# Kernel optimization log

Measured on AMD Instinct MI355X. Metric: run time of the kernel, lower is better.

The kernel has to match this reference:

```python
import jax, jax.numpy as jnp
import numpy as np

NEG_INF = -1e9  # additive mask value for masked softmax


def setup_inputs() -> dict:
    key = jax.random.key(0)
    k1, k2, k3, k4, k5 = jax.random.split(key, 5)
    bz, rv_num, rv_len, in_feat, out_feat = 32, 10, 128, 300, 128
    seq_a = jax.random.normal(k1, (bz, rv_num, rv_len, in_feat), dtype=jnp.float32)
    seq_b = jax.random.normal(k2, (bz, rv_num, rv_len, in_feat), dtype=jnp.float32)
    mask_a = jax.random.randint(k3, (bz, rv_num, rv_len), 0, 2, dtype=jnp.int32)
    mask_b = jax.random.randint(k4, (bz, rv_num, rv_len), 0, 2, dtype=jnp.int32)
    # guarantee at least one valid position per review (avoid fully-masked rows)
    mask_a = mask_a.at[:, :, 0].set(1)
    mask_b = mask_b.at[:, :, 0].set(1)
    # FC transform params (xavier-normal-ish weight, zero bias)
    W = jax.random.normal(k5, (in_feat, out_feat), dtype=jnp.float32) * (2.0 / np.sqrt(in_feat + out_feat))
    b = jnp.zeros((out_feat,), dtype=jnp.float32)
    return {"seq_a": seq_a, "seq_b": seq_b, "mask_a": mask_a, "mask_b": mask_b, "W": W, "b": b}


def _masked_softmax(scores, mask):
    # scores: [N, L], mask: [N, L] in {0,1}
    logits = jnp.where(mask > 0, scores, NEG_INF)
    return jax.nn.softmax(logits, axis=-1)


def reference(seq_a, seq_b, mask_a, mask_b, W, b):
    bz, rv_num, rv_len, _ = seq_a.shape
    hdim = W.shape[1]
    N = bz * rv_num          # flattened batch of reviews
    M = rv_num * rv_len      # all tokens on the other side

    # FC + ReLU feature transform
    ta = jax.nn.relu(jnp.einsum('bnld,dh->bnlh', seq_a, W) + b)
    tb = jax.nn.relu(jnp.einsum('bnld,dh->bnlh', seq_b, W) + b)

    sa = ta.reshape(N, rv_len, hdim)
    sb = tb.reshape(N, rv_len, hdim)
    # expand: each review attends over ALL tokens of the other sequence in its sample
    ea = jnp.broadcast_to(ta.reshape(bz, 1, M, hdim), (bz, rv_num, M, hdim)).reshape(N, M, hdim)
    eb = jnp.broadcast_to(tb.reshape(bz, 1, M, hdim), (bz, rv_num, M, hdim)).reshape(N, M, hdim)

    # DOT interaction (no scale): affinity [N, rv_len, M]
    atob_aff = jnp.einsum('nld,nmd->nlm', sa, eb)
    btoa_aff = jnp.einsum('nld,nmd->nlm', sb, ea)

    # MEAN pooling over the other-sequence axis
    atob_scores = atob_aff.mean(axis=-1)  # [N, rv_len]
    btoa_scores = btoa_aff.mean(axis=-1)

    ma = mask_a.reshape(N, rv_len)
    mb = mask_b.reshape(N, rv_len)
    atob_w = _masked_softmax(atob_scores, ma)
    btoa_w = _masked_softmax(btoa_scores, mb)

    a_out = jnp.einsum('nl,nld->nd', atob_w, sa)
    b_out = jnp.einsum('nl,nld->nd', btoa_w, sb)
    return (a_out, b_out, atob_w, btoa_w)
```

## Files before the change

### kernel.cpp

```cpp
#include <hip/hip_runtime.h>
#include <hip/hip_bf16.h>


#define K_FEAT 300
#define H 128
#define NTOK 40960
#define NREV 320
#define TOK_PER_SAMPLE 1280
#define TM 64
#define FC_BLKS_PER_SIDE 640
#define FC_BLKS_PER_SAMPLE 20
#define NCHUNK 10
#define WFRAG_ELEMS (NCHUNK * 4 * 4 * 64 * 8)

typedef __attribute__((ext_vector_type(8))) short bf16x8;
typedef __attribute__((ext_vector_type(4))) float f32x4;
typedef unsigned short u16;
typedef unsigned int u32;

static __device__ __forceinline__ u16 f2bf(float x) {
    u32 u = __float_as_uint(x);
    return (u16)((u + 0x7fffu + ((u >> 16) & 1u)) >> 16);
}
static __device__ __forceinline__ float bf2f(u16 s) {
    return __uint_as_float(((u32)s) << 16);
}

__global__ void wsplit_kernel(const float* __restrict__ W, u16* __restrict__ Wfrag)
{
    int i = blockIdx.x * 256 + threadIdx.x;
    if (i >= WFRAG_ELEMS) return;
    int j    = i & 7;
    int lane = (i >> 3) & 63;
    int frag = (i >> 9) & 3;
    int wave = (i >> 11) & 3;
    int c    = i >> 13;
    int nn = lane & 15, quad = lane >> 4;
    int t2 = frag >> 1, part = frag & 1;
    int h = (2 * wave + t2) * 16 + nn;
    int k = c * 32 + quad * 8 + j;
    float w = (k < K_FEAT) ? W[(size_t)k * H + h] : 0.f;
    u16 hi = f2bf(w);
    Wfrag[i] = part ? f2bf(w - bf2f(hi)) : hi;
}

static __device__ __forceinline__ void cvt_pack(const float4 a, const float4 b,
                                                uint4& hp, uint4& lp)
{
    u16 h0 = f2bf(a.x), h1 = f2bf(a.y), h2 = f2bf(a.z), h3 = f2bf(a.w);
    u16 h4 = f2bf(b.x), h5 = f2bf(b.y), h6 = f2bf(b.z), h7 = f2bf(b.w);
    hp.x = (u32)h0 | ((u32)h1 << 16);
    hp.y = (u32)h2 | ((u32)h3 << 16);
    hp.z = (u32)h4 | ((u32)h5 << 16);
    hp.w = (u32)h6 | ((u32)h7 << 16);
    lp.x = (u32)f2bf(a.x - bf2f(h0)) | ((u32)f2bf(a.y - bf2f(h1)) << 16);
    lp.y = (u32)f2bf(a.z - bf2f(h2)) | ((u32)f2bf(a.w - bf2f(h3)) << 16);
    lp.z = (u32)f2bf(b.x - bf2f(h4)) | ((u32)f2bf(b.y - bf2f(h5)) << 16);
    lp.w = (u32)f2bf(b.z - bf2f(h6)) | ((u32)f2bf(b.w - bf2f(h7)) << 16);
}

__global__ __launch_bounds__(256, 5) void fc_mfma_kernel(
    const float* __restrict__ seq_a, const float* __restrict__ seq_b,
    const u16* __restrict__ Wfrag, const float* __restrict__ bias,
    u16* __restrict__ ta, u16* __restrict__ tb,
    float* __restrict__ psum_a, float* __restrict__ psum_b)
{
    __shared__ __align__(16) u16 Ah_s[2][4 * 512];
    __shared__ __align__(16) u16 Al_s[2][4 * 512];
    __shared__ float bias_s[H];

    int blk = blockIdx.x;
    const float* seq; u16* outp; float* psum;
    if (blk < FC_BLKS_PER_SIDE) { seq = seq_a; outp = ta; psum = psum_a; }
    else { seq = seq_b; outp = tb; psum = psum_b; blk -= FC_BLKS_PER_SIDE; }

    const int tid = threadIdx.x;
    const int tok0 = blk * TM;
    const int wave = tid >> 6;
    const int lane = tid & 63;
    const int nn = lane & 15;
    const int quad = lane >> 4;

    if (tid < H) bias_s[tid] = bias[tid];

    const int st_tok = tid >> 2;
    const int st_q = tid & 3;
    const float* srow = seq + (size_t)(tok0 + st_tok) * K_FEAT + st_q * 8;
    const int stg = (st_tok >> 4) * 512 + ((st_q << 4) + (st_tok & 15)) * 8;

    f32x4 acc[4][2];
#pragma unroll
    for (int m = 0; m < 4; ++m) {
        acc[m][0] = (f32x4){0.f, 0.f, 0.f, 0.f};
        acc[m][1] = (f32x4){0.f, 0.f, 0.f, 0.f};
    }

#define LOADC(cc, x0, x1) do {                                  \
        int kchk = (cc) * 32 + st_q * 8;                        \
        x0 = make_float4(0.f, 0.f, 0.f, 0.f);                   \
        x1 = make_float4(0.f, 0.f, 0.f, 0.f);                   \
        if (kchk + 4 <= K_FEAT) x0 = *(const float4*)(srow + (cc) * 32);     \
        if (kchk + 8 <= K_FEAT) x1 = *(const float4*)(srow + (cc) * 32 + 4); \
    } while (0)

#define STOREC(bufi, x0, x1) do {                               \
        uint4 hp, lp;                                           \
        cvt_pack(x0, x1, hp, lp);                               \
        *(uint4*)&Ah_s[bufi][stg] = hp;                         \
        *(uint4*)&Al_s[bufi][stg] = lp;                         \
    } while (0)

    float4 a0, a1, b0, b1;
    LOADC(0, a0, a1);
    LOADC(1, b0, b1);
    STOREC(0, a0, a1);
    __syncthreads();

#pragma unroll
    for (int c = 0; c < NCHUNK; ++c) {
        const int cur = c & 1;
        if (c + 2 < NCHUNK) {
            if ((c & 1) == 0) { LOADC(c + 2, a0, a1); }
            else              { LOADC(c + 2, b0, b1); }
        }
        const u16* wf = Wfrag + (size_t)(c * 4 + wave) * 2048;
        bf16x8 bh0 = *(const bf16x8*)&wf[0 * 512 + lane * 8];
        bf16x8 bl0 = *(const bf16x8*)&wf[1 * 512 + lane * 8];
        bf16x8 bh1 = *(const bf16x8*)&wf[2 * 512 + lane * 8];
        bf16x8 bl1 = *(const bf16x8*)&wf[3 * 512 + lane * 8];
#pragma unroll
        for (int m = 0; m < 4; ++m) {
            bf16x8 a_hi = *(const bf16x8*)&Ah_s[cur][m * 512 + lane * 8];
            bf16x8 a_lo = *(const bf16x8*)&Al_s[cur][m * 512 + lane * 8];
            acc[m][0] = __builtin_amdgcn_mfma_f32_16x16x32_bf16(bh0, a_hi, acc[m][0], 0, 0, 0);
            acc[m][0] = __builtin_amdgcn_mfma_f32_16x16x32_bf16(bl0, a_hi, acc[m][0], 0, 0, 0);
            acc[m][0] = __builtin_amdgcn_mfma_f32_16x16x32_bf16(bh0, a_lo, acc[m][0], 0, 0, 0);
            acc[m][1] = __builtin_amdgcn_mfma_f32_16x16x32_bf16(bh1, a_hi, acc[m][1], 0, 0, 0);
            acc[m][1] = __builtin_amdgcn_mfma_f32_16x16x32_bf16(bl1, a_hi, acc[m][1], 0, 0, 0);
            acc[m][1] = __builtin_amdgcn_mfma_f32_16x16x32_bf16(bh1, a_lo, acc[m][1], 0, 0, 0);
        }
        if (c + 1 < NCHUNK) {
            if ((c & 1) == 0) { STOREC(cur ^ 1, b0, b1); }
            else              { STOREC(cur ^ 1, a0, a1); }
            __syncthreads();
        }
    }
#undef LOADC
#undef STOREC

#pragma unroll
    for (int ht = 0; ht < 2; ++ht) {
        int h0 = (2 * wave + ht) * 16 + quad * 4;
        float4 bb = *(const float4*)&bias_s[h0];
        float fs[4] = {0.f, 0.f, 0.f, 0.f};
#pragma unroll
        for (int tt = 0; tt < 4; ++tt) {
            int tok = tok0 + tt * 16 + nn;
            float v0 = fmaxf(acc[tt][ht][0] + bb.x, 0.f);
            float v1 = fmaxf(acc[tt][ht][1] + bb.y, 0.f);
            float v2 = fmaxf(acc[tt][ht][2] + bb.z, 0.f);
            float v3 = fmaxf(acc[tt][ht][3] + bb.w, 0.f);
            fs[0] += v0; fs[1] += v1; fs[2] += v2; fs[3] += v3;
            uint2 p;
            p.x = (u32)f2bf(v0) | ((u32)f2bf(v1) << 16);
            p.y = (u32)f2bf(v2) | ((u32)f2bf(v3) << 16);
            *(uint2*)&outp[(size_t)tok * H + h0] = p;
        }
#pragma unroll
        for (int r = 0; r < 4; ++r) {
            fs[r] += __shfl_xor(fs[r], 1);
            fs[r] += __shfl_xor(fs[r], 2);
            fs[r] += __shfl_xor(fs[r], 4);
            fs[r] += __shfl_xor(fs[r], 8);
        }
        if (nn == 0) {
#pragma unroll
            for (int r = 0; r < 4; ++r)
                psum[(size_t)blk * H + h0 + r] = fs[r];
        }
    }
}

__global__ __launch_bounds__(512) void attn_kernel(
    const u16* __restrict__ ta, const u16* __restrict__ tb,
    const int* __restrict__ mask_a, const int* __restrict__ mask_b,
    const float* __restrict__ psum_a, const float* __restrict__ psum_b,
    float* __restrict__ out)
{
    int n = blockIdx.x;
    int side = 0;
    if (n >= NREV) { side = 1; n -= NREV; }

    const u16* t = side ? tb : ta;
    const int* mask = side ? mask_b : mask_a;
    const float* psum_o = side ? psum_a : psum_b;
    float* out_vec = out + (side ? NREV * H : 0);
    float* out_w = out + 2 * NREV * H + (side ? NREV * H : 0);

    int sample = n / 10;
    int tid = threadIdx.x;

    __shared__ float score_part[128 * 17];
    __shared__ float mean_s[128];
    __shared__ float w_s[128];
    __shared__ float red[8];
    __shared__ float part_out[32 * 128];

    if (tid < 128) {
        float s = 0.f;
        const float* pb = psum_o + (size_t)sample * FC_BLKS_PER_SAMPLE * H + tid;
#pragma unroll
        for (int i = 0; i < FC_BLKS_PER_SAMPLE; ++i) s += pb[(size_t)i * H];
        mean_s[tid] = s * (1.0f / (float)TOK_PER_SAMPLE);
    }
    __syncthreads();

    const u16* rowbase = t + (size_t)n * 128 * H;

#pragma unroll
    for (int i = 0; i < 4; ++i) {
        int q = tid + 512 * i;
        int r = q >> 4;
        int c8 = q & 15;
        uint4 v = *(const uint4*)&rowbase[r * H + c8 * 8];
        const float* m = &mean_s[c8 * 8];
        float p = 0.f;
        p += bf2f((u16)(v.x & 0xffff)) * m[0];
        p += bf2f((u16)(v.x >> 16)) * m[1];
        p += bf2f((u16)(v.y & 0xffff)) * m[2];
        p += bf2f((u16)(v.y >> 16)) * m[3];
        p += bf2f((u16)(v.z & 0xffff)) * m[4];
        p += bf2f((u16)(v.z >> 16)) * m[5];
        p += bf2f((u16)(v.w & 0xffff)) * m[6];
        p += bf2f((u16)(v.w >> 16)) * m[7];
        score_part[r * 17 + c8] = p;
    }
    __syncthreads();

    float logit = -1e9f;
    if (tid < 128) {
        float s = 0.f;
#pragma unroll
        for (int j = 0; j < 16; ++j) s += score_part[tid * 17 + j];
        int mv = mask[n * 128 + tid];
        logit = (mv > 0) ? s : -1e9f;
    }

    float mx = logit;
    for (int off = 32; off > 0; off >>= 1) mx = fmaxf(mx, __shfl_xor(mx, off));
    if ((tid & 63) == 0) red[tid >> 6] = mx;
    __syncthreads();
    mx = red[0];
#pragma unroll
    for (int rr = 1; rr < 8; ++rr) mx = fmaxf(mx, red[rr]);
    __syncthreads();

    float e = __expf(logit - mx);
    float ssum = e;
    for (int off = 32; off > 0; off >>= 1) ssum += __shfl_xor(ssum, off);
    if ((tid & 63) == 0) red[tid >> 6] = ssum;
    __syncthreads();
    ssum = 0.f;
#pragma unroll
    for (int rr = 0; rr < 8; ++rr) ssum += red[rr];

    float w = e / ssum;
    if (tid < 128) {
        w_s[tid] = w;
        out_w[n * 128 + tid] = w;
    }
    __syncthreads();

    int c8 = tid & 15;
    int lp = tid >> 4;
    float o[8] = {0.f, 0.f, 0.f, 0.f, 0.f, 0.f, 0.f, 0.f};
#pragma unroll
    for (int k = 0; k < 4; ++k) {
        int l = k * 32 + lp;
        float wl = w_s[l];
        uint4 v = *(const uint4*)&rowbase[l * H + c8 * 8];
        o[0] = fmaf(wl, bf2f((u16)(v.x & 0xffff)), o[0]);
        o[1] = fmaf(wl, bf2f((u16)(v.x >> 16)), o[1]);
        o[2] = fmaf(wl, bf2f((u16)(v.y & 0xffff)), o[2]);
        o[3] = fmaf(wl, bf2f((u16)(v.y >> 16)), o[3]);
        o[4] = fmaf(wl, bf2f((u16)(v.z & 0xffff)), o[4]);
        o[5] = fmaf(wl, bf2f((u16)(v.z >> 16)), o[5]);
        o[6] = fmaf(wl, bf2f((u16)(v.w & 0xffff)), o[6]);
        o[7] = fmaf(wl, bf2f((u16)(v.w >> 16)), o[7]);
    }
    *(float4*)&part_out[lp * 128 + c8 * 8] = make_float4(o[0], o[1], o[2], o[3]);
    *(float4*)&part_out[lp * 128 + c8 * 8 + 4] = make_float4(o[4], o[5], o[6], o[7]);
    __syncthreads();
    if (tid < 128) {
        float s = 0.f;
#pragma unroll
        for (int p = 0; p < 32; ++p) s += part_out[p * 128 + tid];
        out_vec[n * 128 + tid] = s;
    }
}

extern "C" void kernel_launch(void* const* d_in, const int* in_sizes, int n_in,
                              void* d_out, int out_size, void* d_ws, size_t ws_size,
                              hipStream_t stream)
{
    const float* seq_a = (const float*)d_in[0];
    const float* seq_b = (const float*)d_in[1];
    const int* mask_a = (const int*)d_in[2];
    const int* mask_b = (const int*)d_in[3];
    const float* W = (const float*)d_in[4];
    const float* bias = (const float*)d_in[5];
    float* out = (float*)d_out;

    u16* ta = (u16*)d_ws;
    u16* tb = ta + (size_t)NTOK * H;
    float* psum_a = (float*)(tb + (size_t)NTOK * H);
    float* psum_b = psum_a + FC_BLKS_PER_SIDE * H;
    u16* Wfrag = (u16*)(psum_b + FC_BLKS_PER_SIDE * H);

    wsplit_kernel<<<(WFRAG_ELEMS + 255) / 256, 256, 0, stream>>>(W, Wfrag);
    fc_mfma_kernel<<<2 * FC_BLKS_PER_SIDE, 256, 0, stream>>>(seq_a, seq_b, Wfrag, bias, ta, tb, psum_a, psum_b);
    attn_kernel<<<640, 512, 0, stream>>>(ta, tb, mask_a, mask_b, psum_a, psum_b, out);
}
```

Baseline: 152.8 us.

## Make each FC wave own a private 16-token tile and drop block barriers

The FC kernel now gives each wave its own 16 tokens across all 128 output features, each with private double-buffered LDS staging. This removes every __syncthreads from the K loop. Partial column sums are written per wave, so there are four times as many psum groups, and the attention kernel reduces 80 partials per sample with four accumulators. In exchange, each wave now loads all of the W fragments from global/L2 memory, which is four times the W traffic, and it uses more accumulator registers.

```diff
diff --git a/kernel.cpp b/kernel.cpp
--- a/kernel.cpp
+++ b/kernel.cpp
@@ -9,7 +9,8 @@
 #define TOK_PER_SAMPLE 1280
 #define TM 64
 #define FC_BLKS_PER_SIDE 640
-#define FC_BLKS_PER_SAMPLE 20
+#define PSUM_GROUPS 2560
+#define PSUM_PER_SAMPLE 80
 #define NCHUNK 10
 #define WFRAG_ELEMS (NCHUNK * 4 * 4 * 64 * 8)
 
@@ -33,11 +34,11 @@
     int j    = i & 7;
     int lane = (i >> 3) & 63;
     int frag = (i >> 9) & 3;
-    int wave = (i >> 11) & 3;
+    int p    = (i >> 11) & 3;
     int c    = i >> 13;
     int nn = lane & 15, quad = lane >> 4;
     int t2 = frag >> 1, part = frag & 1;
-    int h = (2 * wave + t2) * 16 + nn;
+    int h = (2 * p + t2) * 16 + nn;
     int k = c * 32 + quad * 8 + j;
     float w = (k < K_FEAT) ? W[(size_t)k * H + h] : 0.f;
     u16 hi = f2bf(w);
@@ -65,9 +66,8 @@
     u16* __restrict__ ta, u16* __restrict__ tb,
     float* __restrict__ psum_a, float* __restrict__ psum_b)
 {
-    __shared__ __align__(16) u16 Ah_s[2][4 * 512];
-    __shared__ __align__(16) u16 Al_s[2][4 * 512];
-    __shared__ float bias_s[H];
+    __shared__ __align__(16) u16 Ah_s[4][2][512];
+    __shared__ __align__(16) u16 Al_s[4][2][512];
 
     int blk = blockIdx.x;
     const float* seq; u16* outp; float* psum;
@@ -75,46 +75,45 @@
     else { seq = seq_b; outp = tb; psum = psum_b; blk -= FC_BLKS_PER_SIDE; }
 
     const int tid = threadIdx.x;
-    const int tok0 = blk * TM;
     const int wave = tid >> 6;
     const int lane = tid & 63;
     const int nn = lane & 15;
     const int quad = lane >> 4;
-
-    if (tid < H) bias_s[tid] = bias[tid];
-
-    const int st_tok = tid >> 2;
-    const int st_q = tid & 3;
-    const float* srow = seq + (size_t)(tok0 + st_tok) * K_FEAT + st_q * 8;
-    const int stg = (st_tok >> 4) * 512 + ((st_q << 4) + (st_tok & 15)) * 8;
-
-    f32x4 acc[4][2];
-#pragma unroll
-    for (int m = 0; m < 4; ++m) {
-        acc[m][0] = (f32x4){0.f, 0.f, 0.f, 0.f};
-        acc[m][1] = (f32x4){0.f, 0.f, 0.f, 0.f};
-    }
-
-#define LOADC(cc, x0, x1) do {                                  \
-        int kchk = (cc) * 32 + st_q * 8;                        \
-        x0 = make_float4(0.f, 0.f, 0.f, 0.f);                   \
-        x1 = make_float4(0.f, 0.f, 0.f, 0.f);                   \
-        if (kchk + 4 <= K_FEAT) x0 = *(const float4*)(srow + (cc) * 32);     \
-        if (kchk + 8 <= K_FEAT) x1 = *(const float4*)(srow + (cc) * 32 + 4); \
+    const int tok0w = blk * TM + wave * 16;
+
+    const int ts = lane >> 2;
+    const int qs = lane & 3;
+    const float* srow = seq + (size_t)(tok0w + ts) * K_FEAT + qs * 8;
+    const int stg = ((qs << 4) + ts) * 8;
+
+    f32x4 acc[8];
+#pragma unroll
+    for (int t = 0; t < 8; ++t) acc[t] = (f32x4){0.f, 0.f, 0.f, 0.f};
+
+#define LOADC(cc, x0, x1) do {                                                \
+        if ((cc) < 9) {   \
+            x0 = *(const float4*)(srow + (cc) * 32);                          \
+            x1 = *(const float4*)(srow + (cc) * 32 + 4);                      \
+        } else {                                                              \
+            int kb = (cc) * 32 + qs * 8;                                      \
+            x0 = make_float4(0.f, 0.f, 0.f, 0.f);                             \
+            x1 = make_float4(0.f, 0.f, 0.f, 0.f);                             \
+            if (kb + 4 <= K_FEAT) x0 = *(const float4*)(srow + (cc) * 32);    \
+            if (kb + 8 <= K_FEAT) x1 = *(const float4*)(srow + (cc) * 32 + 4);\
+        }                                                                     \
     } while (0)
 
 #define STOREC(bufi, x0, x1) do {                               \
         uint4 hp, lp;                                           \
         cvt_pack(x0, x1, hp, lp);                               \
-        *(uint4*)&Ah_s[bufi][stg] = hp;                         \
-        *(uint4*)&Al_s[bufi][stg] = lp;                         \
+        *(uint4*)&Ah_s[wave][bufi][stg] = hp;                   \
+        *(uint4*)&Al_s[wave][bufi][stg] = lp;                   \
     } while (0)
 
     float4 a0, a1, b0, b1;
     LOADC(0, a0, a1);
     LOADC(1, b0, b1);
     STOREC(0, a0, a1);
-    __syncthreads();
 
 #pragma unroll
     for (int c = 0; c < NCHUNK; ++c) {
@@ -123,60 +122,57 @@
             if ((c & 1) == 0) { LOADC(c + 2, a0, a1); }
             else              { LOADC(c + 2, b0, b1); }
         }
-        const u16* wf = Wfrag + (size_t)(c * 4 + wave) * 2048;
-        bf16x8 bh0 = *(const bf16x8*)&wf[0 * 512 + lane * 8];
-        bf16x8 bl0 = *(const bf16x8*)&wf[1 * 512 + lane * 8];
-        bf16x8 bh1 = *(const bf16x8*)&wf[2 * 512 + lane * 8];
-        bf16x8 bl1 = *(const bf16x8*)&wf[3 * 512 + lane * 8];
-#pragma unroll
-        for (int m = 0; m < 4; ++m) {
-            bf16x8 a_hi = *(const bf16x8*)&Ah_s[cur][m * 512 + lane * 8];
-            bf16x8 a_lo = *(const bf16x8*)&Al_s[cur][m * 512 + lane * 8];
-            acc[m][0] = __builtin_amdgcn_mfma_f32_16x16x32_bf16(bh0, a_hi, acc[m][0], 0, 0, 0);
-            acc[m][0] = __builtin_amdgcn_mfma_f32_16x16x32_bf16(bl0, a_hi, acc[m][0], 0, 0, 0);
-            acc[m][0] = __builtin_amdgcn_mfma_f32_16x16x32_bf16(bh0, a_lo, acc[m][0], 0, 0, 0);
-            acc[m][1] = __builtin_amdgcn_mfma_f32_16x16x32_bf16(bh1, a_hi, acc[m][1], 0, 0, 0);
-            acc[m][1] = __builtin_amdgcn_mfma_f32_16x16x32_bf16(bl1, a_hi, acc[m][1], 0, 0, 0);
-            acc[m][1] = __builtin_amdgcn_mfma_f32_16x16x32_bf16(bh1, a_lo, acc[m][1], 0, 0, 0);
-        }
+        bf16x8 a_hi = *(const bf16x8*)&Ah_s[wave][cur][lane * 8];
+        bf16x8 a_lo = *(const bf16x8*)&Al_s[wave][cur][lane * 8];
         if (c + 1 < NCHUNK) {
             if ((c & 1) == 0) { STOREC(cur ^ 1, b0, b1); }
             else              { STOREC(cur ^ 1, a0, a1); }
-            __syncthreads();
+        }
+        const u16* wfc = Wfrag + (size_t)c * 8192;
+#pragma unroll
+        for (int p = 0; p < 4; ++p) {
+            const u16* wf = wfc + p * 2048;
+            bf16x8 bh0 = *(const bf16x8*)&wf[0 * 512 + lane * 8];
+            bf16x8 bl0 = *(const bf16x8*)&wf[1 * 512 + lane * 8];
+            bf16x8 bh1 = *(const bf16x8*)&wf[2 * 512 + lane * 8];
+            bf16x8 bl1 = *(const bf16x8*)&wf[3 * 512 + lane * 8];
+            acc[2 * p]     = __builtin_amdgcn_mfma_f32_16x16x32_bf16(bh0, a_hi, acc[2 * p], 0, 0, 0);
+            acc[2 * p]     = __builtin_amdgcn_mfma_f32_16x16x32_bf16(bl0, a_hi, acc[2 * p], 0, 0, 0);
+            acc[2 * p]     = __builtin_amdgcn_mfma_f32_16x16x32_bf16(bh0, a_lo, acc[2 * p], 0, 0, 0);
+            acc[2 * p + 1] = __builtin_amdgcn_mfma_f32_16x16x32_bf16(bh1, a_hi, acc[2 * p + 1], 0, 0, 0);
+            acc[2 * p + 1] = __builtin_amdgcn_mfma_f32_16x16x32_bf16(bl1, a_hi, acc[2 * p + 1], 0, 0, 0);
+            acc[2 * p + 1] = __builtin_amdgcn_mfma_f32_16x16x32_bf16(bh1, a_lo, acc[2 * p + 1], 0, 0, 0);
         }
     }
 #undef LOADC
 #undef STOREC
 
-#pragma unroll
-    for (int ht = 0; ht < 2; ++ht) {
-        int h0 = (2 * wave + ht) * 16 + quad * 4;
-        float4 bb = *(const float4*)&bias_s[h0];
-        float fs[4] = {0.f, 0.f, 0.f, 0.f};
-#pragma unroll
-        for (int tt = 0; tt < 4; ++tt) {
-            int tok = tok0 + tt * 16 + nn;
-            float v0 = fmaxf(acc[tt][ht][0] + bb.x, 0.f);
-            float v1 = fmaxf(acc[tt][ht][1] + bb.y, 0.f);
-            float v2 = fmaxf(acc[tt][ht][2] + bb.z, 0.f);
-            float v3 = fmaxf(acc[tt][ht][3] + bb.w, 0.f);
-            fs[0] += v0; fs[1] += v1; fs[2] += v2; fs[3] += v3;
-            uint2 p;
-            p.x = (u32)f2bf(v0) | ((u32)f2bf(v1) << 16);
-            p.y = (u32)f2bf(v2) | ((u32)f2bf(v3) << 16);
-            *(uint2*)&outp[(size_t)tok * H + h0] = p;
-        }
-#pragma unroll
-        for (int r = 0; r < 4; ++r) {
-            fs[r] += __shfl_xor(fs[r], 1);
-            fs[r] += __shfl_xor(fs[r], 2);
-            fs[r] += __shfl_xor(fs[r], 4);
-            fs[r] += __shfl_xor(fs[r], 8);
+    const int g = blk * 4 + wave;
+#pragma unroll
+    for (int ht = 0; ht < 8; ++ht) {
+        const int h0 = ht * 16 + quad * 4;
+        const float4 bb = *(const float4*)&bias[h0];
+        float v0 = fmaxf(acc[ht][0] + bb.x, 0.f);
+        float v1 = fmaxf(acc[ht][1] + bb.y, 0.f);
+        float v2 = fmaxf(acc[ht][2] + bb.z, 0.f);
+        float v3 = fmaxf(acc[ht][3] + bb.w, 0.f);
+        uint2 pk;
+        pk.x = (u32)f2bf(v0) | ((u32)f2bf(v1) << 16);
+        pk.y = (u32)f2bf(v2) | ((u32)f2bf(v3) << 16);
+        *(uint2*)&outp[(size_t)(tok0w + nn) * H + h0] = pk;
+        float fs0 = v0, fs1 = v1, fs2 = v2, fs3 = v3;
+#pragma unroll
+        for (int x = 1; x < 16; x <<= 1) {
+            fs0 += __shfl_xor(fs0, x);
+            fs1 += __shfl_xor(fs1, x);
+            fs2 += __shfl_xor(fs2, x);
+            fs3 += __shfl_xor(fs3, x);
         }
         if (nn == 0) {
-#pragma unroll
-            for (int r = 0; r < 4; ++r)
-                psum[(size_t)blk * H + h0 + r] = fs[r];
+            psum[(size_t)g * H + h0 + 0] = fs0;
+            psum[(size_t)g * H + h0 + 1] = fs1;
+            psum[(size_t)g * H + h0 + 2] = fs2;
+            psum[(size_t)g * H + h0 + 3] = fs3;
         }
     }
 }
@@ -207,11 +203,16 @@
     __shared__ float part_out[32 * 128];
 
     if (tid < 128) {
-        float s = 0.f;
-        const float* pb = psum_o + (size_t)sample * FC_BLKS_PER_SAMPLE * H + tid;
-#pragma unroll
-        for (int i = 0; i < FC_BLKS_PER_SAMPLE; ++i) s += pb[(size_t)i * H];
-        mean_s[tid] = s * (1.0f / (float)TOK_PER_SAMPLE);
+        const float* pb = psum_o + (size_t)sample * PSUM_PER_SAMPLE * H + tid;
+        float s0 = 0.f, s1 = 0.f, s2 = 0.f, s3 = 0.f;
+#pragma unroll
+        for (int i = 0; i < PSUM_PER_SAMPLE; i += 4) {
+            s0 += pb[(size_t)(i + 0) * H];
+            s1 += pb[(size_t)(i + 1) * H];
+            s2 += pb[(size_t)(i + 2) * H];
+            s3 += pb[(size_t)(i + 3) * H];
+        }
+        mean_s[tid] = (s0 + s1 + s2 + s3) * (1.0f / (float)TOK_PER_SAMPLE);
     }
     __syncthreads();
 
@@ -314,8 +315,8 @@
     u16* ta = (u16*)d_ws;
     u16* tb = ta + (size_t)NTOK * H;
     float* psum_a = (float*)(tb + (size_t)NTOK * H);
-    float* psum_b = psum_a + FC_BLKS_PER_SIDE * H;
-    u16* Wfrag = (u16*)(psum_b + FC_BLKS_PER_SIDE * H);
+    float* psum_b = psum_a + PSUM_GROUPS * H;
+    u16* Wfrag = (u16*)(psum_b + PSUM_GROUPS * H);
 
     wsplit_kernel<<<(WFRAG_ELEMS + 255) / 256, 256, 0, stream>>>(W, Wfrag);
     fc_mfma_kernel<<<2 * FC_BLKS_PER_SIDE, 256, 0, stream>>>(seq_a, seq_b, Wfrag, bias, ta, tb, psum_a, psum_b);
```

After: 190.8 us. +24.9%, slower.

## Replace split-bf16 triple MFMA with single fp16 MFMA; cache rows in LDS

Applied to the files above, without the earlier changes.

The FC GEMM drops the hi/lo bf16 split, which took three MFMAs per tile, and instead converts activations and weights to fp16 for a single f16 MFMA. This cuts MFMA count, LDS traffic and conversion work, at the cost of fp16 precision and range on the inputs. The load prefetch depth drops from two chunks to one, and bias is read from global memory directly. The attention kernel now stages each review's token rows in LDS on the first pass so the second pass reads LDS instead of global memory, and it reuses one float buffer for both reduction scratch arrays.

```diff
diff --git a/kernel.cpp b/kernel.cpp
--- a/kernel.cpp
+++ b/kernel.cpp
@@ -11,9 +11,10 @@
 #define FC_BLKS_PER_SIDE 640
 #define FC_BLKS_PER_SAMPLE 20
 #define NCHUNK 10
-#define WFRAG_ELEMS (NCHUNK * 4 * 4 * 64 * 8)
-
-typedef __attribute__((ext_vector_type(8))) short bf16x8;
+#define WFRAG_ELEMS (NCHUNK * 4 * 2 * 64 * 8)
+
+typedef _Float16 f16;
+typedef __attribute__((ext_vector_type(8))) _Float16 f16x8;
 typedef __attribute__((ext_vector_type(4))) float f32x4;
 typedef unsigned short u16;
 typedef unsigned int u32;
@@ -24,6 +25,13 @@
 }
 static __device__ __forceinline__ float bf2f(u16 s) {
     return __uint_as_float(((u32)s) << 16);
+}
+static __device__ __forceinline__ u16 f2h_bits(float x) {
+    f16 h = (f16)x;
+    return *(u16*)&h;
+}
+static __device__ __forceinline__ u32 pk2h(float a, float b) {
+    return (u32)f2h_bits(a) | ((u32)f2h_bits(b) << 16);
 }
 
 __global__ void wsplit_kernel(const float* __restrict__ W, u16* __restrict__ Wfrag)
@@ -32,31 +40,14 @@
     if (i >= WFRAG_ELEMS) return;
     int j    = i & 7;
     int lane = (i >> 3) & 63;
-    int frag = (i >> 9) & 3;
-    int wave = (i >> 11) & 3;
-    int c    = i >> 13;
+    int t2   = (i >> 9) & 1;
+    int p    = (i >> 10) & 3;
+    int c    = i >> 12;
     int nn = lane & 15, quad = lane >> 4;
-    int t2 = frag >> 1, part = frag & 1;
-    int h = (2 * wave + t2) * 16 + nn;
+    int h = (2 * p + t2) * 16 + nn;
     int k = c * 32 + quad * 8 + j;
     float w = (k < K_FEAT) ? W[(size_t)k * H + h] : 0.f;
-    u16 hi = f2bf(w);
-    Wfrag[i] = part ? f2bf(w - bf2f(hi)) : hi;
-}
-
-static __device__ __forceinline__ void cvt_pack(const float4 a, const float4 b,
-                                                uint4& hp, uint4& lp)
-{
-    u16 h0 = f2bf(a.x), h1 = f2bf(a.y), h2 = f2bf(a.z), h3 = f2bf(a.w);
-    u16 h4 = f2bf(b.x), h5 = f2bf(b.y), h6 = f2bf(b.z), h7 = f2bf(b.w);
-    hp.x = (u32)h0 | ((u32)h1 << 16);
-    hp.y = (u32)h2 | ((u32)h3 << 16);
-    hp.z = (u32)h4 | ((u32)h5 << 16);
-    hp.w = (u32)h6 | ((u32)h7 << 16);
-    lp.x = (u32)f2bf(a.x - bf2f(h0)) | ((u32)f2bf(a.y - bf2f(h1)) << 16);
-    lp.y = (u32)f2bf(a.z - bf2f(h2)) | ((u32)f2bf(a.w - bf2f(h3)) << 16);
-    lp.z = (u32)f2bf(b.x - bf2f(h4)) | ((u32)f2bf(b.y - bf2f(h5)) << 16);
-    lp.w = (u32)f2bf(b.z - bf2f(h6)) | ((u32)f2bf(b.w - bf2f(h7)) << 16);
+    Wfrag[i] = f2h_bits(w);
 }
 
 __global__ __launch_bounds__(256, 5) void fc_mfma_kernel(
@@ -65,9 +56,7 @@
     u16* __restrict__ ta, u16* __restrict__ tb,
     float* __restrict__ psum_a, float* __restrict__ psum_b)
 {
-    __shared__ __align__(16) u16 Ah_s[2][4 * 512];
-    __shared__ __align__(16) u16 Al_s[2][4 * 512];
-    __shared__ float bias_s[H];
+    __shared__ __align__(16) u16 A_s[2][4 * 512];
 
     int blk = blockIdx.x;
     const float* seq; u16* outp; float* psum;
@@ -81,8 +70,6 @@
     const int nn = lane & 15;
     const int quad = lane >> 4;
 
-    if (tid < H) bias_s[tid] = bias[tid];
-
     const int st_tok = tid >> 2;
     const int st_q = tid & 3;
     const float* srow = seq + (size_t)(tok0 + st_tok) * K_FEAT + st_q * 8;
@@ -95,53 +82,48 @@
         acc[m][1] = (f32x4){0.f, 0.f, 0.f, 0.f};
     }
 
-#define LOADC(cc, x0, x1) do {                                  \
-        int kchk = (cc) * 32 + st_q * 8;                        \
-        x0 = make_float4(0.f, 0.f, 0.f, 0.f);                   \
-        x1 = make_float4(0.f, 0.f, 0.f, 0.f);                   \
-        if (kchk + 4 <= K_FEAT) x0 = *(const float4*)(srow + (cc) * 32);     \
-        if (kchk + 8 <= K_FEAT) x1 = *(const float4*)(srow + (cc) * 32 + 4); \
+#define LOADC(cc, x0, x1) do {                                                \
+        if ((cc) < 9) {        \
+            x0 = *(const float4*)(srow + (cc) * 32);                          \
+            x1 = *(const float4*)(srow + (cc) * 32 + 4);                      \
+        } else {                                                              \
+            int kb = (cc) * 32 + st_q * 8;                                    \
+            x0 = make_float4(0.f, 0.f, 0.f, 0.f);                             \
+            x1 = make_float4(0.f, 0.f, 0.f, 0.f);                             \
+            if (kb + 4 <= K_FEAT) x0 = *(const float4*)(srow + (cc) * 32);    \
+            if (kb + 8 <= K_FEAT) x1 = *(const float4*)(srow + (cc) * 32 + 4);\
+        }                                                                     \
     } while (0)
 
 #define STOREC(bufi, x0, x1) do {                               \
-        uint4 hp, lp;                                           \
-        cvt_pack(x0, x1, hp, lp);                               \
-        *(uint4*)&Ah_s[bufi][stg] = hp;                         \
-        *(uint4*)&Al_s[bufi][stg] = lp;                         \
+        uint4 pkt;                                              \
+        pkt.x = pk2h(x0.x, x0.y);                               \
+        pkt.y = pk2h(x0.z, x0.w);                               \
+        pkt.z = pk2h(x1.x, x1.y);                               \
+        pkt.w = pk2h(x1.z, x1.w);                               \
+        *(uint4*)&A_s[bufi][stg] = pkt;                         \
     } while (0)
 
-    float4 a0, a1, b0, b1;
-    LOADC(0, a0, a1);
-    LOADC(1, b0, b1);
-    STOREC(0, a0, a1);
+    float4 x0, x1;
+    LOADC(0, x0, x1);
+    STOREC(0, x0, x1);
     __syncthreads();
 
 #pragma unroll
     for (int c = 0; c < NCHUNK; ++c) {
         const int cur = c & 1;
-        if (c + 2 < NCHUNK) {
-            if ((c & 1) == 0) { LOADC(c + 2, a0, a1); }
-            else              { LOADC(c + 2, b0, b1); }
-        }
-        const u16* wf = Wfrag + (size_t)(c * 4 + wave) * 2048;
-        bf16x8 bh0 = *(const bf16x8*)&wf[0 * 512 + lane * 8];
-        bf16x8 bl0 = *(const bf16x8*)&wf[1 * 512 + lane * 8];
-        bf16x8 bh1 = *(const bf16x8*)&wf[2 * 512 + lane * 8];
-        bf16x8 bl1 = *(const bf16x8*)&wf[3 * 512 + lane * 8];
+        if (c + 1 < NCHUNK) LOADC(c + 1, x0, x1);
+        const u16* wf = Wfrag + (size_t)c * 4096 + (size_t)wave * 1024;
+        f16x8 wh0 = *(const f16x8*)&wf[0 * 512 + lane * 8];
+        f16x8 wh1 = *(const f16x8*)&wf[1 * 512 + lane * 8];
 #pragma unroll
         for (int m = 0; m < 4; ++m) {
-            bf16x8 a_hi = *(const bf16x8*)&Ah_s[cur][m * 512 + lane * 8];
-            bf16x8 a_lo = *(const bf16x8*)&Al_s[cur][m * 512 + lane * 8];
-            acc[m][0] = __builtin_amdgcn_mfma_f32_16x16x32_bf16(bh0, a_hi, acc[m][0], 0, 0, 0);
-            acc[m][0] = __builtin_amdgcn_mfma_f32_16x16x32_bf16(bl0, a_hi, acc[m][0], 0, 0, 0);
-            acc[m][0] = __builtin_amdgcn_mfma_f32_16x16x32_bf16(bh0, a_lo, acc[m][0], 0, 0, 0);
-            acc[m][1] = __builtin_amdgcn_mfma_f32_16x16x32_bf16(bh1, a_hi, acc[m][1], 0, 0, 0);
-            acc[m][1] = __builtin_amdgcn_mfma_f32_16x16x32_bf16(bl1, a_hi, acc[m][1], 0, 0, 0);
-            acc[m][1] = __builtin_amdgcn_mfma_f32_16x16x32_bf16(bh1, a_lo, acc[m][1], 0, 0, 0);
+            f16x8 a = *(const f16x8*)&A_s[cur][m * 512 + lane * 8];
+            acc[m][0] = __builtin_amdgcn_mfma_f32_16x16x32_f16(wh0, a, acc[m][0], 0, 0, 0);
+            acc[m][1] = __builtin_amdgcn_mfma_f32_16x16x32_f16(wh1, a, acc[m][1], 0, 0, 0);
         }
         if (c + 1 < NCHUNK) {
-            if ((c & 1) == 0) { STOREC(cur ^ 1, b0, b1); }
-            else              { STOREC(cur ^ 1, a0, a1); }
+            STOREC(cur ^ 1, x0, x1);
             __syncthreads();
         }
     }
@@ -150,21 +132,21 @@
 
 #pragma unroll
     for (int ht = 0; ht < 2; ++ht) {
-        int h0 = (2 * wave + ht) * 16 + quad * 4;
-        float4 bb = *(const float4*)&bias_s[h0];
+        const int h0 = (2 * wave + ht) * 16 + quad * 4;
+        const float4 bb = *(const float4*)&bias[h0];
         float fs[4] = {0.f, 0.f, 0.f, 0.f};
 #pragma unroll
-        for (int tt = 0; tt < 4; ++tt) {
-            int tok = tok0 + tt * 16 + nn;
-            float v0 = fmaxf(acc[tt][ht][0] + bb.x, 0.f);
-            float v1 = fmaxf(acc[tt][ht][1] + bb.y, 0.f);
-            float v2 = fmaxf(acc[tt][ht][2] + bb.z, 0.f);
-            float v3 = fmaxf(acc[tt][ht][3] + bb.w, 0.f);
+        for (int m = 0; m < 4; ++m) {
+            int tok = tok0 + m * 16 + nn;
+            float v0 = fmaxf(acc[m][ht][0] + bb.x, 0.f);
+            float v1 = fmaxf(acc[m][ht][1] + bb.y, 0.f);
+            float v2 = fmaxf(acc[m][ht][2] + bb.z, 0.f);
+            float v3 = fmaxf(acc[m][ht][3] + bb.w, 0.f);
             fs[0] += v0; fs[1] += v1; fs[2] += v2; fs[3] += v3;
-            uint2 p;
-            p.x = (u32)f2bf(v0) | ((u32)f2bf(v1) << 16);
-            p.y = (u32)f2bf(v2) | ((u32)f2bf(v3) << 16);
-            *(uint2*)&outp[(size_t)tok * H + h0] = p;
+            uint2 pk;
+            pk.x = (u32)f2bf(v0) | ((u32)f2bf(v1) << 16);
+            pk.y = (u32)f2bf(v2) | ((u32)f2bf(v3) << 16);
+            *(uint2*)&outp[(size_t)tok * H + h0] = pk;
         }
 #pragma unroll
         for (int r = 0; r < 4; ++r) {
@@ -200,11 +182,11 @@
     int sample = n / 10;
     int tid = threadIdx.x;
 
-    __shared__ float score_part[128 * 17];
+    __shared__ __align__(16) u16 T_s[128 * 128];
+    __shared__ float fbuf[32 * 128];
     __shared__ float mean_s[128];
     __shared__ float w_s[128];
     __shared__ float red[8];
-    __shared__ float part_out[32 * 128];
 
     if (tid < 128) {
         float s = 0.f;
@@ -223,6 +205,7 @@
         int r = q >> 4;
         int c8 = q & 15;
         uint4 v = *(const uint4*)&rowbase[r * H + c8 * 8];
+        *(uint4*)&T_s[r * H + c8 * 8] = v;
         const float* m = &mean_s[c8 * 8];
         float p = 0.f;
         p += bf2f((u16)(v.x & 0xffff)) * m[0];
@@ -233,7 +216,7 @@
         p += bf2f((u16)(v.z >> 16)) * m[5];
         p += bf2f((u16)(v.w & 0xffff)) * m[6];
         p += bf2f((u16)(v.w >> 16)) * m[7];
-        score_part[r * 17 + c8] = p;
+        fbuf[r * 17 + c8] = p;
     }
     __syncthreads();
 
@@ -241,7 +224,7 @@
     if (tid < 128) {
         float s = 0.f;
 #pragma unroll
-        for (int j = 0; j < 16; ++j) s += score_part[tid * 17 + j];
+        for (int j = 0; j < 16; ++j) s += fbuf[tid * 17 + j];
         int mv = mask[n * 128 + tid];
         logit = (mv > 0) ? s : -1e9f;
     }
@@ -278,7 +261,7 @@
     for (int k = 0; k < 4; ++k) {
         int l = k * 32 + lp;
         float wl = w_s[l];
-        uint4 v = *(const uint4*)&rowbase[l * H + c8 * 8];
+        uint4 v = *(const uint4*)&T_s[l * H + c8 * 8];
         o[0] = fmaf(wl, bf2f((u16)(v.x & 0xffff)), o[0]);
         o[1] = fmaf(wl, bf2f((u16)(v.x >> 16)), o[1]);
         o[2] = fmaf(wl, bf2f((u16)(v.y & 0xffff)), o[2]);
@@ -288,13 +271,13 @@
         o[6] = fmaf(wl, bf2f((u16)(v.w & 0xffff)), o[6]);
         o[7] = fmaf(wl, bf2f((u16)(v.w >> 16)), o[7]);
     }
-    *(float4*)&part_out[lp * 128 + c8 * 8] = make_float4(o[0], o[1], o[2], o[3]);
-    *(float4*)&part_out[lp * 128 + c8 * 8 + 4] = make_float4(o[4], o[5], o[6], o[7]);
+    *(float4*)&fbuf[lp * 128 + c8 * 8] = make_float4(o[0], o[1], o[2], o[3]);
+    *(float4*)&fbuf[lp * 128 + c8 * 8 + 4] = make_float4(o[4], o[5], o[6], o[7]);
     __syncthreads();
     if (tid < 128) {
         float s = 0.f;
 #pragma unroll
-        for (int p = 0; p < 32; ++p) s += part_out[p * 128 + tid];
+        for (int p = 0; p < 32; ++p) s += fbuf[p * 128 + tid];
         out_vec[n * 128 + tid] = s;
     }
 }
```

New measurement: 151.5 us. About the same (-0.9%).
